# Kernel optimization log

Hardware: AMD Instinct MI355X
Metric: run time of the kernel (lower is better)

Reference implementation:

```python
import jax, jax.numpy as jnp
import numpy as np
from jax import lax

I, H, B, T = 2048, 96, 64, 512

def _rnn_layer(x_in, w_ih, b_ih, w_hh, b_hh):
    """One tanh-RNN layer. x_in: [B, T, D]. Returns [B, T, H]."""
    # Hoist the big input GEMM out of the scan (one batched matmul).
    xproj = jnp.einsum('btd,hd->bth', x_in, w_ih) + b_ih  # [B, T, H]
    def step(h, xt):  # h: [B, H], xt: [B, H]
        h = jnp.tanh(xt + h @ w_hh.T + b_hh)
        return h, h
    h0 = jnp.zeros((x_in.shape[0], w_hh.shape[0]), dtype=x_in.dtype)
    _, ys = lax.scan(step, h0, jnp.swapaxes(xproj, 0, 1))  # [T, B, H]
    return jnp.swapaxes(ys, 0, 1)

def setup_inputs() -> dict:
    key = jax.random.key(0)
    ks = jax.random.split(key, 12)
    s = 0.05  # keep pre-activations in tanh's linear-ish range
    x = jax.random.normal(ks[0], (B, T, I), dtype=jnp.float32)
    return {
        'x': x,
        'w_ih0': jax.random.normal(ks[1], (H, I), jnp.float32) * s,
        'w_hh0': jax.random.normal(ks[2], (H, H), jnp.float32) * s,
        'b_ih0': jnp.zeros((H,), jnp.float32),
        'b_hh0': jnp.zeros((H,), jnp.float32),
        'w_ih1': jax.random.normal(ks[3], (H, H), jnp.float32) * s,
        'w_hh1': jax.random.normal(ks[4], (H, H), jnp.float32) * s,
        'b_ih1': jnp.zeros((H,), jnp.float32),
        'b_hh1': jnp.zeros((H,), jnp.float32),
        'w_ih2': jax.random.normal(ks[5], (H, H), jnp.float32) * s,
        'w_hh2': jax.random.normal(ks[6], (H, H), jnp.float32) * s,
        'b_ih2': jnp.zeros((H,), jnp.float32),
        'b_hh2': jnp.zeros((H,), jnp.float32),
        'fc_w': jax.random.normal(ks[7], (1, H), jnp.float32) * s,
        'fc_b': jnp.zeros((1,), jnp.float32),
    }

def reference(x, w_ih0, w_hh0, b_ih0, b_hh0,
              w_ih1, w_hh1, b_ih1, b_hh1,
              w_ih2, w_hh2, b_ih2, b_hh2,
              fc_w, fc_b):
    # 3-layer tanh RNN (eval mode: inter-layer dropout p=0.1 and head dropout
    # p=0.2 are identity), then last-timestep linear head.
    h1 = _rnn_layer(x,  w_ih0, b_ih0, w_hh0, b_hh0)  # [B, T, H]
    h2 = _rnn_layer(h1, w_ih1, b_ih1, w_hh1, b_hh1)
    h3 = _rnn_layer(h2, w_ih2, b_ih2, w_hh2, b_hh2)
    last = h3[:, -1, :]                               # [B, H]
    return last @ fc_w.T + fc_b                       # [B, 1]
```

## Files before the change

kernel.cpp:

```cpp
#include <hip/hip_runtime.h>
#include <hip/hip_bf16.h>

#define T_STEPS 512
#define B_SZ 64
#define H_SZ 96
#define I_SZ 2048

#define BM 64
#define BN 96
#define BK 32

typedef const __attribute__((address_space(1))) void g_void;
typedef __attribute__((address_space(3))) void l_void;

__device__ __forceinline__ void stage_tile(const float* __restrict__ x,
                                           const float* __restrict__ w,
                                           float* xsf, float* wsf,
                                           int buf, int m0, int k0, int tid) {
#pragma unroll
    for (int it = 0; it < 2; ++it) {
        int L = tid + it * 256;
        int m = L >> 3;
        int c = (L & 7) ^ ((L >> 5) & 7);
        const float* g = &x[(size_t)(m0 + m) * I_SZ + k0 + c * 4];
        __builtin_amdgcn_global_load_lds((g_void*)g,
            (l_void*)(xsf + buf * (BM * BK) + L * 4), 16, 0, 0);
    }
#pragma unroll
    for (int it = 0; it < 3; ++it) {
        int L = tid + it * 256;
        int j = L >> 3;
        int c = (L & 7) ^ ((L >> 5) & 7);
        const float* g = &w[(size_t)j * I_SZ + k0 + c * 4];
        __builtin_amdgcn_global_load_lds((g_void*)g,
            (l_void*)(wsf + buf * (BN * BK) + L * 4), 16, 0, 0);
    }
}

__global__ __launch_bounds__(256) void xproj_gemm(
    const float* __restrict__ x,
    const float* __restrict__ w,
    const float* __restrict__ bias,
    float* __restrict__ out)
{
    __shared__ __align__(16) float xsf[2 * BM * BK];
    __shared__ __align__(16) float wsf[2 * BN * BK];

    const int tid = threadIdx.x;
    const int m0 = blockIdx.x * BM;
    const int tm = tid & 15;
    const int tn = tid >> 4;

    float bb[6];
#pragma unroll
    for (int c = 0; c < 6; ++c) bb[c] = bias[tn * 6 + c];

    int aoff[4], boff[6], sb[6];
    const int sa = tm & 7;
#pragma unroll
    for (int r = 0; r < 4; ++r) aoff[r] = (tm * 4 + r) * 8;
#pragma unroll
    for (int c = 0; c < 6; ++c) {
        int j = tn * 6 + c;
        boff[c] = j * 8;
        sb[c] = (j >> 2) & 7;
    }

    float acc[4][6];
#pragma unroll
    for (int r = 0; r < 4; ++r)
#pragma unroll
        for (int c = 0; c < 6; ++c) acc[r][c] = 0.f;

    stage_tile(x, w, xsf, wsf, 0, m0, 0, tid);
    __syncthreads();

    for (int tile = 0; tile < I_SZ / BK; ++tile) {
        const int buf = tile & 1;
        if (tile < I_SZ / BK - 1)
            stage_tile(x, w, xsf, wsf, buf ^ 1, m0, (tile + 1) * BK, tid);

        const float4* xsb = (const float4*)(xsf + buf * (BM * BK));
        const float4* wsb = (const float4*)(wsf + buf * (BN * BK));
#pragma unroll
        for (int cc = 0; cc < 8; ++cc) {
            float av[4][4], bv[6][4];
#pragma unroll
            for (int r = 0; r < 4; ++r)
                *(float4*)av[r] = xsb[aoff[r] + (cc ^ sa)];
#pragma unroll
            for (int c = 0; c < 6; ++c)
                *(float4*)bv[c] = wsb[boff[c] + (cc ^ sb[c])];
#pragma unroll
            for (int kk = 0; kk < 4; ++kk)
#pragma unroll
                for (int r = 0; r < 4; ++r)
#pragma unroll
                    for (int c = 0; c < 6; ++c)
                        acc[r][c] = fmaf(av[r][kk], bv[c][kk], acc[r][c]);
        }
        __syncthreads();
    }

#pragma unroll
    for (int r = 0; r < 4; ++r) {
        float* op = &out[(size_t)(m0 + tm * 4 + r) * H_SZ + tn * 6];
        *(float2*)(op + 0) = make_float2(acc[r][0] + bb[0], acc[r][1] + bb[1]);
        *(float2*)(op + 2) = make_float2(acc[r][2] + bb[2], acc[r][3] + bb[3]);
        *(float2*)(op + 4) = make_float2(acc[r][4] + bb[4], acc[r][5] + bb[5]);
    }
}


#define WQ_LIST(F) \
    F(0,0) F(0,1) F(0,2) F(0,3) F(0,4) F(0,5) \
    F(1,0) F(1,1) F(1,2) F(1,3) F(1,4) F(1,5) \
    F(2,0) F(2,1) F(2,2) F(2,3) F(2,4) F(2,5) \
    F(3,0) F(3,1) F(3,2) F(3,3) F(3,4) F(3,5)

__device__ __forceinline__ float fast_tanh(float x) {
    float cx = fminf(fmaxf(x, -15.f), 15.f);
    float e = __expf(2.f * cx);
    return 1.f - 2.f / (e + 1.f);
}

#define CHUNK 256

__global__ __launch_bounds__(512, 2) void rnn3_fused(
    const float* __restrict__ xproj0,
    const float* __restrict__ w_hh0, const float* __restrict__ b_hh0,
    const float* __restrict__ w_ih1, const float* __restrict__ b_ih1,
    const float* __restrict__ w_hh1, const float* __restrict__ b_hh1,
    const float* __restrict__ w_ih2, const float* __restrict__ b_ih2,
    const float* __restrict__ w_hh2, const float* __restrict__ b_hh2,
    const float* __restrict__ fc_w, const float* __restrict__ fc_b,
    float* __restrict__ out)
{
    __shared__ __align__(16) float xp_ch[CHUNK * H_SZ];
    __shared__ __align__(16) float hls[2 * 3 * H_SZ];
    __shared__ float red[H_SZ];

    const int t = threadIdx.x;
    const int b = blockIdx.x;
    const int wv = t >> 6;
    const int l = t & 63;

    int half, q, sub, j0, in_sel, out_sel, layer;
    const float* mat;
    if (wv < 6) {
        half = l >> 5; int lq = l & 31; q = lq >> 2; sub = lq & 3;
        if (wv < 3) { layer = 1; j0 = wv * 32 + q * 4;
                      mat = half ? w_hh1 : w_ih1; in_sel = half ? 1 : 0; out_sel = 1; }
        else        { layer = 2; j0 = (wv - 3) * 32 + q * 4;
                      mat = half ? w_hh2 : w_ih2; in_sel = half ? 2 : 1; out_sel = 2; }
    } else {
        half = 0; q = l >> 2; sub = l & 3; layer = 0;
        j0 = (wv - 6) * 64 + q * 4;
        mat = w_hh0; in_sel = 0; out_sel = 0;
    }
    const bool jvalid = (j0 < H_SZ);
    const int j0c = jvalid ? j0 : H_SZ - 4;
    const int jme = j0c + sub;
    const float* wrb = mat + j0c * H_SZ + sub * 24;

#define DECLW(r, c) float4 W##r##_##c = *(const float4*)(wrb + (r) * H_SZ + (c) * 4);
    WQ_LIST(DECLW)

    float cb;
    if (layer == 0)      cb = b_hh0[jme];
    else if (layer == 1) cb = b_ih1[jme] + b_hh1[jme];
    else                 cb = b_ih2[jme] + b_hh2[jme];

    for (int k = t; k < 2 * 3 * H_SZ; k += 512) hls[k] = 0.f;
    __syncthreads();

    const float* xp_base = xproj0 + (size_t)b * T_STEPS * H_SZ;

    for (int i = 0; i < T_STEPS + 2; ++i) {
        if ((i & (CHUNK - 1)) == 0 && i < T_STEPS) {
            const float4* src = (const float4*)(xp_base + (size_t)i * H_SZ);
            float4* dst = (float4*)xp_ch;
#pragma unroll
            for (int qq = 0; qq < 12; ++qq) dst[t + qq * 512] = src[t + qq * 512];
            __syncthreads();
        }
        const int buf = i & 1;

        const float4* hp = (const float4*)&hls[buf * (3 * H_SZ) + in_sel * H_SZ + sub * 24];
        float4 hv0 = hp[0], hv1 = hp[1], hv2 = hp[2], hv3 = hp[3], hv4 = hp[4], hv5 = hp[5];

        float xpv = 0.f;
        if (layer == 0) xpv = xp_ch[(i & (CHUNK - 1)) * H_SZ + jme];

        float a0 = 0.f, a1 = 0.f, a2 = 0.f, a3 = 0.f;
#define DOTQ(r, c) { a##r = fmaf(W##r##_##c.x, hv##c.x, a##r); \
                     a##r = fmaf(W##r##_##c.y, hv##c.y, a##r); \
                     a##r = fmaf(W##r##_##c.z, hv##c.z, a##r); \
                     a##r = fmaf(W##r##_##c.w, hv##c.w, a##r); }
        WQ_LIST(DOTQ)

        float m0 = (sub & 1) ? a0 : a1;
        float m1 = (sub & 1) ? a2 : a3;
        float x0 = __shfl_xor(m0, 1, 64);
        float x1 = __shfl_xor(m1, 1, 64);
        float u0 = ((sub & 1) ? a1 : a0) + x0;
        float u1 = ((sub & 1) ? a3 : a2) + x1;
        float m2 = (sub & 2) ? u0 : u1;
        float x2 = __shfl_xor(m2, 2, 64);
        float fin = ((sub & 2) ? u1 : u0) + x2;

        float fin2 = fin + __shfl_xor(fin, 32, 64);

        float* hn = &hls[(buf ^ 1) * (3 * H_SZ) + out_sel * H_SZ];
        if (layer == 0) {
            if (jvalid && i < T_STEPS) hn[jme] = fast_tanh(fin + xpv + cb);
        } else if (half == 0) {
            bool ok = (layer == 1) ? (i >= 1 && i <= T_STEPS) : (i >= 2);
            if (ok) hn[jme] = fast_tanh(fin2 + cb);
        }
        __syncthreads();
    }

    if (t < H_SZ) red[t] = hls[2 * H_SZ + t] * fc_w[t];
    __syncthreads();
    if (t == 0) {
        float sm = 0.f;
#pragma unroll
        for (int k = 0; k < H_SZ; ++k) sm += red[k];
        out[b] = sm + fc_b[0];
    }
}

extern "C" void kernel_launch(void* const* d_in, const int* in_sizes, int n_in,
                              void* d_out, int out_size, void* d_ws, size_t ws_size,
                              hipStream_t stream) {
    const float* x     = (const float*)d_in[0];
    const float* w_ih0 = (const float*)d_in[1];
    const float* w_hh0 = (const float*)d_in[2];
    const float* b_ih0 = (const float*)d_in[3];
    const float* b_hh0 = (const float*)d_in[4];
    const float* w_ih1 = (const float*)d_in[5];
    const float* w_hh1 = (const float*)d_in[6];
    const float* b_ih1 = (const float*)d_in[7];
    const float* b_hh1 = (const float*)d_in[8];
    const float* w_ih2 = (const float*)d_in[9];
    const float* w_hh2 = (const float*)d_in[10];
    const float* b_ih2 = (const float*)d_in[11];
    const float* b_hh2 = (const float*)d_in[12];
    const float* fc_w  = (const float*)d_in[13];
    const float* fc_b  = (const float*)d_in[14];

    float* xproj = (float*)d_ws;

    const int M = B_SZ * T_STEPS;
    xproj_gemm<<<M / BM, 256, 0, stream>>>(x, w_ih0, b_ih0, xproj);
    rnn3_fused<<<B_SZ, 512, 0, stream>>>(xproj,
                                         w_hh0, b_hh0,
                                         w_ih1, b_ih1, w_hh1, b_hh1,
                                         w_ih2, b_ih2, w_hh2, b_hh2,
                                         fc_w, fc_b, (float*)d_out);
}
```

Measured before the change: 837.9 us.

## Pipeline RNN layers as per-wave chunked stages with LDS ring buffers

Restructures the fused 3-layer RNN kernel so that each layer's serial recurrence runs in a single wavefront. Each wave holds that layer's full W_hh rows in registers and syncs only within the wave (via LDS) for PP=8 timesteps per chunk. The input projections for layers 1 and 2 are computed in bulk by separate waves one chunk behind, and another wave prefetches xproj0 chunks, with block barriers only once per chunk instead of every timestep. This cuts the per-step __syncthreads cost and shortens the critical path, but the serial waves rely on intra-wave LDS ordering without explicit barriers and carry heavier register pressure (48 float4).

```diff
diff --git a/kernel.cpp b/kernel.cpp
--- a/kernel.cpp
+++ b/kernel.cpp
@@ -112,11 +112,10 @@
 }
 
 
-#define WQ_LIST(F) \
-    F(0,0) F(0,1) F(0,2) F(0,3) F(0,4) F(0,5) \
-    F(1,0) F(1,1) F(1,2) F(1,3) F(1,4) F(1,5) \
-    F(2,0) F(2,1) F(2,2) F(2,3) F(2,4) F(2,5) \
-    F(3,0) F(3,1) F(3,2) F(3,3) F(3,4) F(3,5)
+#define PP 8
+#define RING 32
+#define NCH (T_STEPS / PP)
+#define NPER (NCH + 4)
 
 __device__ __forceinline__ float fast_tanh(float x) {
     float cx = fminf(fmaxf(x, -15.f), 15.f);
@@ -124,7 +123,70 @@
     return 1.f - 2.f / (e + 1.f);
 }
 
-#define CHUNK 256
+__device__ __forceinline__ void serial_chunk(
+    float4 (&R)[48], float cb0, float cb1, float cb2,
+    float* __restrict__ ringS, const float* __restrict__ ihsrc,
+    int tb, int p, int kh)
+{
+    const int j0 = 3 * p;
+    const int hbase = kh * 48;
+#pragma unroll
+    for (int i8 = 0; i8 < PP; ++i8) {
+        const int sofs = ((tb + i8) & (RING - 1)) * H_SZ;
+        float id0 = ihsrc[i8 * H_SZ + j0 + 0];
+        float id1 = ihsrc[i8 * H_SZ + j0 + 1];
+        float id2 = ihsrc[i8 * H_SZ + j0 + 2];
+        float a0x = 0.f, a0y = 0.f, a0z = 0.f, a0w = 0.f;
+        float a1x = 0.f, a1y = 0.f, a1z = 0.f, a1w = 0.f;
+        float a2x = 0.f, a2y = 0.f, a2z = 0.f, a2w = 0.f;
+#pragma unroll
+        for (int c = 0; c < 12; ++c) {
+            float4 h = R[36 + c];
+            a0x = fmaf(R[c].x,      h.x, a0x); a0y = fmaf(R[c].y,      h.y, a0y);
+            a0z = fmaf(R[c].z,      h.z, a0z); a0w = fmaf(R[c].w,      h.w, a0w);
+            a1x = fmaf(R[12 + c].x, h.x, a1x); a1y = fmaf(R[12 + c].y, h.y, a1y);
+            a1z = fmaf(R[12 + c].z, h.z, a1z); a1w = fmaf(R[12 + c].w, h.w, a1w);
+            a2x = fmaf(R[24 + c].x, h.x, a2x); a2y = fmaf(R[24 + c].y, h.y, a2y);
+            a2z = fmaf(R[24 + c].z, h.z, a2z); a2w = fmaf(R[24 + c].w, h.w, a2w);
+        }
+        float a0 = (a0x + a0y) + (a0z + a0w);
+        float a1 = (a1x + a1y) + (a1z + a1w);
+        float a2 = (a2x + a2y) + (a2z + a2w);
+        a0 += __shfl_xor(a0, 1, 64);
+        a1 += __shfl_xor(a1, 1, 64);
+        a2 += __shfl_xor(a2, 1, 64);
+        float h0v = fast_tanh(a0 + id0 + cb0);
+        float h1v = fast_tanh(a1 + id1 + cb1);
+        float h2v = fast_tanh(a2 + id2 + cb2);
+        if (kh == 0) {
+            ringS[sofs + j0 + 0] = h0v;
+            ringS[sofs + j0 + 1] = h1v;
+        } else {
+            ringS[sofs + j0 + 2] = h2v;
+        }
+#pragma unroll
+        for (int c = 0; c < 12; ++c)
+            R[36 + c] = *(const float4*)&ringS[sofs + hbase + c * 4];
+    }
+}
+
+__device__ __forceinline__ void bulk_chunk(
+    float4 (&R)[48], const float* __restrict__ ringSrc,
+    float* __restrict__ dst, int tb, int row, bool act)
+{
+#pragma unroll
+    for (int i8 = 0; i8 < PP; ++i8) {
+        const int sofs = ((tb + i8) & (RING - 1)) * H_SZ;
+        float ax = 0.f, ay = 0.f, az = 0.f, aw = 0.f;
+#pragma unroll
+        for (int c = 0; c < 24; ++c) {
+            float4 h = *(const float4*)&ringSrc[sofs + c * 4];
+            ax = fmaf(R[c].x, h.x, ax); ay = fmaf(R[c].y, h.y, ay);
+            az = fmaf(R[c].z, h.z, az); aw = fmaf(R[c].w, h.w, aw);
+        }
+        if (act) dst[i8 * H_SZ + row] = (ax + ay) + (az + aw);
+    }
+}
 
 __global__ __launch_bounds__(512, 2) void rnn3_fused(
     const float* __restrict__ xproj0,
@@ -136,92 +198,110 @@
     const float* __restrict__ fc_w, const float* __restrict__ fc_b,
     float* __restrict__ out)
 {
-    __shared__ __align__(16) float xp_ch[CHUNK * H_SZ];
-    __shared__ __align__(16) float hls[2 * 3 * H_SZ];
+    __shared__ __align__(16) float ring0[RING * H_SZ];
+    __shared__ __align__(16) float ring1[RING * H_SZ];
+    __shared__ __align__(16) float ring2[RING * H_SZ];
+    __shared__ __align__(16) float ihd1[2][PP * H_SZ];
+    __shared__ __align__(16) float ihd2[2][PP * H_SZ];
+    __shared__ __align__(16) float xpb[2][PP * H_SZ];
     __shared__ float red[H_SZ];
 
     const int t = threadIdx.x;
     const int b = blockIdx.x;
     const int wv = t >> 6;
     const int l = t & 63;
-
-    int half, q, sub, j0, in_sel, out_sel, layer;
-    const float* mat;
-    if (wv < 6) {
-        half = l >> 5; int lq = l & 31; q = lq >> 2; sub = lq & 3;
-        if (wv < 3) { layer = 1; j0 = wv * 32 + q * 4;
-                      mat = half ? w_hh1 : w_ih1; in_sel = half ? 1 : 0; out_sel = 1; }
-        else        { layer = 2; j0 = (wv - 3) * 32 + q * 4;
-                      mat = half ? w_hh2 : w_ih2; in_sel = half ? 2 : 1; out_sel = 2; }
+    const int p = l >> 1, kh = l & 1;
+
+    for (int k = t; k < RING * H_SZ; k += 512) {
+        ring0[k] = 0.f; ring1[k] = 0.f; ring2[k] = 0.f;
+    }
+
+    const float* xp_base = xproj0 + (size_t)b * T_STEPS * H_SZ;
+
+    float4 R[48];
+    float cb0 = 0.f, cb1 = 0.f, cb2 = 0.f;
+    int rowid = 0;
+    bool rowact = false;
+
+    if (wv < 3) {
+        const float* wm = (wv == 0) ? w_hh0 : (wv == 1 ? w_hh1 : w_hh2);
+        const int j0 = 3 * p;
+#pragma unroll
+        for (int r = 0; r < 3; ++r)
+#pragma unroll
+            for (int c = 0; c < 12; ++c)
+                R[r * 12 + c] = *(const float4*)&wm[(j0 + r) * H_SZ + kh * 48 + c * 4];
+#pragma unroll
+        for (int c = 0; c < 12; ++c) R[36 + c] = make_float4(0.f, 0.f, 0.f, 0.f);
+        if (wv == 0) {
+            cb0 = b_hh0[j0]; cb1 = b_hh0[j0 + 1]; cb2 = b_hh0[j0 + 2];
+        } else if (wv == 1) {
+            cb0 = b_ih1[j0]     + b_hh1[j0];
+            cb1 = b_ih1[j0 + 1] + b_hh1[j0 + 1];
+            cb2 = b_ih1[j0 + 2] + b_hh1[j0 + 2];
+        } else {
+            cb0 = b_ih2[j0]     + b_hh2[j0];
+            cb1 = b_ih2[j0 + 1] + b_hh2[j0 + 1];
+            cb2 = b_ih2[j0 + 2] + b_hh2[j0 + 2];
+        }
+        __builtin_amdgcn_s_setprio(1);
+    } else if (wv == 3 || wv == 4) {
+        int rr = (wv - 3) * 64 + l;
+        rowact = rr < H_SZ; rowid = rowact ? rr : (H_SZ - 1);
+#pragma unroll
+        for (int c = 0; c < 24; ++c)
+            R[c] = *(const float4*)&w_ih1[rowid * H_SZ + c * 4];
+    } else if (wv >= 6) {
+        int rr = (wv - 6) * 64 + l;
+        rowact = rr < H_SZ; rowid = rowact ? rr : (H_SZ - 1);
+#pragma unroll
+        for (int c = 0; c < 24; ++c)
+            R[c] = *(const float4*)&w_ih2[rowid * H_SZ + c * 4];
     } else {
-        half = 0; q = l >> 2; sub = l & 3; layer = 0;
-        j0 = (wv - 6) * 64 + q * 4;
-        mat = w_hh0; in_sel = 0; out_sel = 0;
-    }
-    const bool jvalid = (j0 < H_SZ);
-    const int j0c = jvalid ? j0 : H_SZ - 4;
-    const int jme = j0c + sub;
-    const float* wrb = mat + j0c * H_SZ + sub * 24;
-
-#define DECLW(r, c) float4 W##r##_##c = *(const float4*)(wrb + (r) * H_SZ + (c) * 4);
-    WQ_LIST(DECLW)
-
-    float cb;
-    if (layer == 0)      cb = b_hh0[jme];
-    else if (layer == 1) cb = b_ih1[jme] + b_hh1[jme];
-    else                 cb = b_ih2[jme] + b_hh2[jme];
-
-    for (int k = t; k < 2 * 3 * H_SZ; k += 512) hls[k] = 0.f;
+#pragma unroll
+        for (int q = 0; q < 3; ++q) {
+            int idx = (l + 64 * q) * 4;
+            *(float4*)&xpb[0][idx] = *(const float4*)&xp_base[idx];
+        }
+    }
     __syncthreads();
 
-    const float* xp_base = xproj0 + (size_t)b * T_STEPS * H_SZ;
-
-    for (int i = 0; i < T_STEPS + 2; ++i) {
-        if ((i & (CHUNK - 1)) == 0 && i < T_STEPS) {
-            const float4* src = (const float4*)(xp_base + (size_t)i * H_SZ);
-            float4* dst = (float4*)xp_ch;
-#pragma unroll
-            for (int qq = 0; qq < 12; ++qq) dst[t + qq * 512] = src[t + qq * 512];
-            __syncthreads();
-        }
-        const int buf = i & 1;
-
-        const float4* hp = (const float4*)&hls[buf * (3 * H_SZ) + in_sel * H_SZ + sub * 24];
-        float4 hv0 = hp[0], hv1 = hp[1], hv2 = hp[2], hv3 = hp[3], hv4 = hp[4], hv5 = hp[5];
-
-        float xpv = 0.f;
-        if (layer == 0) xpv = xp_ch[(i & (CHUNK - 1)) * H_SZ + jme];
-
-        float a0 = 0.f, a1 = 0.f, a2 = 0.f, a3 = 0.f;
-#define DOTQ(r, c) { a##r = fmaf(W##r##_##c.x, hv##c.x, a##r); \
-                     a##r = fmaf(W##r##_##c.y, hv##c.y, a##r); \
-                     a##r = fmaf(W##r##_##c.z, hv##c.z, a##r); \
-                     a##r = fmaf(W##r##_##c.w, hv##c.w, a##r); }
-        WQ_LIST(DOTQ)
-
-        float m0 = (sub & 1) ? a0 : a1;
-        float m1 = (sub & 1) ? a2 : a3;
-        float x0 = __shfl_xor(m0, 1, 64);
-        float x1 = __shfl_xor(m1, 1, 64);
-        float u0 = ((sub & 1) ? a1 : a0) + x0;
-        float u1 = ((sub & 1) ? a3 : a2) + x1;
-        float m2 = (sub & 2) ? u0 : u1;
-        float x2 = __shfl_xor(m2, 2, 64);
-        float fin = ((sub & 2) ? u1 : u0) + x2;
-
-        float fin2 = fin + __shfl_xor(fin, 32, 64);
-
-        float* hn = &hls[(buf ^ 1) * (3 * H_SZ) + out_sel * H_SZ];
-        if (layer == 0) {
-            if (jvalid && i < T_STEPS) hn[jme] = fast_tanh(fin + xpv + cb);
-        } else if (half == 0) {
-            bool ok = (layer == 1) ? (i >= 1 && i <= T_STEPS) : (i >= 2);
-            if (ok) hn[jme] = fast_tanh(fin2 + cb);
+    for (int m = 0; m < NPER; ++m) {
+        if (wv == 0) {
+            if (m < NCH)
+                serial_chunk(R, cb0, cb1, cb2, ring0, &xpb[m & 1][0], m * PP, p, kh);
+        } else if (wv == 1) {
+            int cc = m - 2;
+            if (cc >= 0 && cc < NCH)
+                serial_chunk(R, cb0, cb1, cb2, ring1, &ihd1[cc & 1][0], cc * PP, p, kh);
+        } else if (wv == 2) {
+            int cc = m - 4;
+            if (cc >= 0 && cc < NCH)
+                serial_chunk(R, cb0, cb1, cb2, ring2, &ihd2[cc & 1][0], cc * PP, p, kh);
+        } else if (wv == 3 || wv == 4) {
+            int cc = m - 1;
+            if (cc >= 0 && cc < NCH)
+                bulk_chunk(R, ring0, &ihd1[cc & 1][0], cc * PP, rowid, rowact);
+        } else if (wv == 5) {
+            int cs = m + 1;
+            if (cs < NCH) {
+                const float* src = xp_base + (size_t)cs * PP * H_SZ;
+                float* dstx = &xpb[cs & 1][0];
+#pragma unroll
+                for (int q = 0; q < 3; ++q) {
+                    int idx = (l + 64 * q) * 4;
+                    *(float4*)&dstx[idx] = *(const float4*)&src[idx];
+                }
+            }
+        } else {
+            int cc = m - 3;
+            if (cc >= 0 && cc < NCH)
+                bulk_chunk(R, ring1, &ihd2[cc & 1][0], cc * PP, rowid, rowact);
         }
         __syncthreads();
     }
 
-    if (t < H_SZ) red[t] = hls[2 * H_SZ + t] * fc_w[t];
+    if (t < H_SZ) red[t] = ring2[((T_STEPS - 1) & (RING - 1)) * H_SZ + t] * fc_w[t];
     __syncthreads();
     if (t == 0) {
         float sm = 0.f;
```

After: 1.150 ms. 37.2% more time.
